# Kernel optimization log

Hardware: AMD Instinct MI355X
Metric: run time of the kernel (lower is better)

The kernel has to match this reference:

```python
import jax, jax.numpy as jnp
import numpy as np

S = 2048      # sequence length (prefill, start_idx=0)
D = 4096      # model dim
H = 32        # query heads
KVH = 8       # kv heads (GQA)
HD = D // H   # head dim = 128
ROPE_BASE = 500000.0  # llama3 rope theta
NEG = -1e9    # additive causal mask value (finite stand-in for -inf)


def setup_inputs() -> dict:
    key = jax.random.key(0)
    ks = jax.random.split(key, 5)
    scale = 1.0 / np.sqrt(D)
    x = jax.random.normal(ks[0], (S, D), jnp.float32)
    wq = jax.random.normal(ks[1], (D, D), jnp.float32) * scale
    wk = jax.random.normal(ks[2], (KVH * HD, D), jnp.float32) * scale
    wv = jax.random.normal(ks[3], (KVH * HD, D), jnp.float32) * scale
    wo = jax.random.normal(ks[4], (D, D), jnp.float32) * scale
    # RoPE tables, [S, HD//2]
    pos = jnp.arange(S, dtype=jnp.float32)
    inv_freq = 1.0 / (ROPE_BASE ** (jnp.arange(0, HD, 2, dtype=jnp.float32) / HD))
    ang = pos[:, None] * inv_freq[None, :]
    freqs_cos = jnp.cos(ang)
    freqs_sin = jnp.sin(ang)
    # additive causal mask [S, S]
    mask = jnp.where(jnp.tril(jnp.ones((S, S), bool)), 0.0, NEG).astype(jnp.float32)
    return dict(x=x, wq=wq, wk=wk, wv=wv, wo=wo, mask=mask,
                freqs_cos=freqs_cos, freqs_sin=freqs_sin)


def _rope(t, cos, sin):
    # t: [S, nh, hd]; cos/sin: [S, hd//2] -> interleaved even/odd rotation
    even = t[:, :, 0::2]
    odd = t[:, :, 1::2]
    c = cos[:, None, :]
    s = sin[:, None, :]
    re = even * c - odd * s
    im = even * s + odd * c
    return jnp.stack([re, im], axis=-1).reshape(t.shape)


def reference(x, wq, wk, wv, wo, mask, freqs_cos, freqs_sin):
    s, d = x.shape
    q = (x @ wq.T).reshape(s, H, HD)
    k = (x @ wk.T).reshape(s, KVH, HD)
    v = (x @ wv.T).reshape(s, KVH, HD)
    q = _rope(q, freqs_cos, freqs_sin)
    k = _rope(k, freqs_cos, freqs_sin)
    # KV-cache append at start_idx=0 then read back == identity (prefill)
    # GQA: repeat_interleave kv heads to match query heads
    k = jnp.repeat(k, H // KVH, axis=1)  # [s, H, HD]
    v = jnp.repeat(v, H // KVH, axis=1)
    logits = jnp.einsum('qhd,khd->hqk', q, k) * (1.0 / np.sqrt(HD)) + mask[None]
    p = jax.nn.softmax(logits, axis=-1)
    o = jnp.einsum('hqk,khd->qhd', p, v).reshape(s, d)
    return o @ wo.T
```

## Files before the change

### kernel.cpp

```cpp
#include <hip/hip_runtime.h>
#include <hip/hip_bf16.h>
#include <stdint.h>

#define S2   2048
#define DD   4096
#define NH   32
#define NKVH 8
#define HD2  128
#define QKVW 6144

typedef __bf16 bf16x8 __attribute__((ext_vector_type(8)));
typedef float  f32x4  __attribute__((ext_vector_type(4)));
typedef unsigned short u16x8 __attribute__((ext_vector_type(8)));
typedef unsigned short u16x4 __attribute__((ext_vector_type(4)));

__device__ __forceinline__ unsigned short f2b(float f) {
    unsigned int u = __builtin_bit_cast(unsigned int, f);
    unsigned int r = (u + 0x7FFFu + ((u >> 16) & 1u)) >> 16;
    return (unsigned short)r;
}
__device__ __forceinline__ float b2f(unsigned short h) {
    unsigned int u = ((unsigned int)h) << 16;
    return __builtin_bit_cast(float, u);
}
__device__ __forceinline__ unsigned cvt_pk_bf16(float a, float b) {
    unsigned r;
    asm("v_cvt_pk_bf16_f32 %0, %1, %2" : "=v"(r) : "v"(a), "v"(b));
    return r;
}

__device__ __forceinline__ void gload_lds16(const void* g, void* lds) {
    __builtin_amdgcn_global_load_lds(
        (const __attribute__((address_space(1))) void*)(uintptr_t)g,
        (__attribute__((address_space(3))) void*)(uint32_t)(uintptr_t)lds,
        16, 0, 0);
}

#define BAR() do { asm volatile("" ::: "memory"); \
                   __builtin_amdgcn_s_barrier();  \
                   asm volatile("" ::: "memory"); } while (0)
#define WAITV(n) asm volatile("s_waitcnt vmcnt(" #n ")" ::: "memory")

template<int N> __device__ __forceinline__ void waitv() {
    if      constexpr (N == 0)  WAITV(0);
    else if constexpr (N == 1)  WAITV(1);
    else if constexpr (N == 2)  WAITV(2);
    else if constexpr (N == 3)  WAITV(3);
    else if constexpr (N == 4)  WAITV(4);
    else if constexpr (N == 5)  WAITV(5);
    else if constexpr (N == 6)  WAITV(6);
    else if constexpr (N == 8)  WAITV(8);
}

__global__ void cvt_all(const float* __restrict__ x,  const float* __restrict__ wq,
                        const float* __restrict__ wk, const float* __restrict__ wv,
                        const float* __restrict__ wo, unsigned short* __restrict__ dst) {
    const long long NG = 12LL * 1024 * 1024;
    const long long stride = (long long)gridDim.x * blockDim.x;
    for (long long g = (long long)blockIdx.x * blockDim.x + threadIdx.x; g < NG; g += stride) {
        const float* src; long long off;
        if      (g < 2LL*1024*1024) { src = x;  off = g; }
        else if (g < 6LL*1024*1024) { src = wq; off = g - 2LL*1024*1024; }
        else if (g < 7LL*1024*1024) { src = wk; off = g - 6LL*1024*1024; }
        else if (g < 8LL*1024*1024) { src = wv; off = g - 7LL*1024*1024; }
        else                        { src = wo; off = g - 8LL*1024*1024; }
        f32x4 v = *reinterpret_cast<const f32x4*>(src + off * 4);
        u16x4 o;
        o[0] = f2b(v[0]); o[1] = f2b(v[1]); o[2] = f2b(v[2]); o[3] = f2b(v[3]);
        *reinterpret_cast<u16x4*>(dst + g * 4) = o;
    }
}

__global__ __launch_bounds__(512) void gemm_qkv(
    const unsigned short* __restrict__ A,
    const unsigned short* __restrict__ B0,
    const unsigned short* __restrict__ B1,
    const unsigned short* __restrict__ B2,
    unsigned short* __restrict__ C)
{
    constexpr int K = 4096, BK = 64, NT = K / BK;
    __shared__ unsigned short As[2][256 * 64];
    __shared__ unsigned short Bs[2][192 * 64];

    const int bm = blockIdx.y, bn = blockIdx.x;
    const int tid = threadIdx.x;
    const int w = tid >> 6, lane = tid & 63;
    const int wr = w >> 1, wc = w & 1;
    const int r16 = lane & 15, g4 = lane >> 4;

    const int bn0 = bn * 192;
    const unsigned short* Ap = A + (size_t)bm * 256 * K;

    const int lrow = lane >> 3;
    const int lchk = lane & 7;

    f32x4 acc[4][6] = {};
    bf16x8 af[2][2], b0[3][2], b1[3][2];

    auto browbase = [&](int rowg) -> const unsigned short* {
        if (rowg < 4096) return B0 + (size_t)rowg * K;
        if (rowg < 5120) return B1 + (size_t)(rowg - 4096) * K;
        return B2 + (size_t)(rowg - 5120) * K;
    };

    auto stageA = [&](int buf, int tt, int half) {
        #pragma unroll
        for (int i = 0; i < 2; ++i) {
            const int j = i * 8 + w;
            const int row0 = (j >> 2) * 64 + half * 32 + (j & 3) * 8;
            const int row = row0 + lrow;
            gload_lds16(Ap + (size_t)row * K + tt * BK + ((lchk ^ (row & 7)) * 8),
                        &As[buf][row0 * 64]);
        }
    };
    auto stageB = [&](int buf, int tt, int half) {
        #pragma unroll
        for (int i = 0; i < 2; ++i) {
            const int j = (i == 0) ? w : (8 + (w & 3));
            const int row0 = (j < 6) ? (half * 48 + j * 8)
                                     : (96 + half * 48 + (j - 6) * 8);
            const int row = row0 + lrow;
            const unsigned short* src = browbase(bn0 + row0) + (size_t)lrow * K;
            gload_lds16(src + tt * BK + ((lchk ^ (row & 7)) * 8),
                        &Bs[buf][row0 * 64]);
        }
    };
    auto readA = [&](int buf, int mh) {
        #pragma unroll
        for (int m = 0; m < 2; ++m)
            #pragma unroll
            for (int kk = 0; kk < 2; ++kk) {
                const int row = wr * 64 + mh * 32 + m * 16 + r16;
                af[m][kk] = *reinterpret_cast<const bf16x8*>(
                    &As[buf][row * 64 + (((kk * 4 + g4) ^ (row & 7)) * 8)]);
            }
    };
    auto readB = [&](int buf, int nh, bf16x8 (&br)[3][2]) {
        #pragma unroll
        for (int n = 0; n < 3; ++n)
            #pragma unroll
            for (int kk = 0; kk < 2; ++kk) {
                const int row = wc * 96 + nh * 48 + n * 16 + r16;
                br[n][kk] = *reinterpret_cast<const bf16x8*>(
                    &Bs[buf][row * 64 + (((kk * 4 + g4) ^ (row & 7)) * 8)]);
            }
    };
    auto mma = [&](bf16x8 (&br)[3][2], int mh, int nh) {
        __builtin_amdgcn_s_setprio(1);
        #pragma unroll
        for (int m = 0; m < 2; ++m)
            #pragma unroll
            for (int n = 0; n < 3; ++n)
                #pragma unroll
                for (int kk = 0; kk < 2; ++kk)
                    acc[mh * 2 + m][nh * 3 + n] = __builtin_amdgcn_mfma_f32_16x16x32_bf16(
                        af[m][kk], br[n][kk], acc[mh * 2 + m][nh * 3 + n], 0, 0, 0);
        __builtin_amdgcn_s_setprio(0);
    };

    stageA(0, 0, 0); stageB(0, 0, 0); stageB(0, 0, 1); stageA(0, 0, 1);
    waitv<4>();
    BAR();

    for (int t = 0; t < NT - 1; ++t) {
        const int buf = t & 1;
        readA(buf, 0); readB(buf, 0, b0);
        stageA(buf ^ 1, t + 1, 0); stageB(buf ^ 1, t + 1, 0);
        BAR();
        mma(b0, 0, 0);
        waitv<6>();
        BAR();
        readB(buf, 1, b1);
        stageB(buf ^ 1, t + 1, 1);
        BAR();
        mma(b1, 0, 1);
        waitv<6>();
        BAR();
        readA(buf, 1);
        stageA(buf ^ 1, t + 1, 1);
        BAR();
        mma(b1, 1, 1);
        BAR();
        mma(b0, 1, 0);
        waitv<4>();
        BAR();
    }
    {
        const int buf = (NT - 1) & 1;
        readA(buf, 0); readB(buf, 0, b0);
        BAR();
        mma(b0, 0, 0);
        waitv<2>();
        BAR();
        readB(buf, 1, b1);
        mma(b1, 0, 1);
        waitv<0>();
        readA(buf, 1);
        mma(b1, 1, 1);
        mma(b0, 1, 0);
    }

    const size_t crow0 = (size_t)bm * 256 + wr * 64;
    const size_t ccol0 = (size_t)bn0 + wc * 96;
    #pragma unroll
    for (int m = 0; m < 4; ++m)
        #pragma unroll
        for (int n = 0; n < 6; ++n)
            #pragma unroll
            for (int r = 0; r < 4; ++r)
                C[(crow0 + m * 16 + g4 * 4 + r) * QKVW + ccol0 + n * 16 + r16] =
                    f2b(acc[m][n][r]);
}

__global__ __launch_bounds__(512) void gemm_out(
    const unsigned short* __restrict__ A,
    const unsigned short* __restrict__ B,
    float* __restrict__ C)
{
    constexpr int K = 4096, BK = 64, NT = K / BK;
    __shared__ unsigned short As[2][128 * 64];
    __shared__ unsigned short Bs[2][256 * 64];

    const int bm = blockIdx.y, bn = blockIdx.x;
    const int tid = threadIdx.x;
    const int w = tid >> 6, lane = tid & 63;
    const int wr = w >> 2, wc = w & 3;
    const int r16 = lane & 15, g4 = lane >> 4;

    const unsigned short* Ap = A + (size_t)bm * 128 * K;
    const unsigned short* Bp = B + (size_t)bn * 256 * K;

    const int lrow = lane >> 3;
    const int lchk = lane & 7;

    f32x4 acc[4][4] = {};
    bf16x8 af[2][2], b0[2][2], b1[2][2];

    auto stageA = [&](int buf, int tt, int half) {
        const int j = w;
        const int row0 = (j >> 2) * 64 + half * 32 + (j & 3) * 8;
        const int row = row0 + lrow;
        gload_lds16(Ap + (size_t)row * K + tt * BK + ((lchk ^ (row & 7)) * 8),
                    &As[buf][row0 * 64]);
    };
    auto stageB = [&](int buf, int tt, int half) {
        #pragma unroll
        for (int i = 0; i < 2; ++i) {
            const int j = i * 8 + w;
            const int row0 = (j >> 2) * 64 + half * 32 + (j & 3) * 8;
            const int row = row0 + lrow;
            gload_lds16(Bp + (size_t)row * K + tt * BK + ((lchk ^ (row & 7)) * 8),
                        &Bs[buf][row0 * 64]);
        }
    };
    auto readA = [&](int buf, int mh) {
        #pragma unroll
        for (int m = 0; m < 2; ++m)
            #pragma unroll
            for (int kk = 0; kk < 2; ++kk) {
                const int row = wr * 64 + mh * 32 + m * 16 + r16;
                af[m][kk] = *reinterpret_cast<const bf16x8*>(
                    &As[buf][row * 64 + (((kk * 4 + g4) ^ (row & 7)) * 8)]);
            }
    };
    auto readB = [&](int buf, int nh, bf16x8 (&br)[2][2]) {
        #pragma unroll
        for (int n = 0; n < 2; ++n)
            #pragma unroll
            for (int kk = 0; kk < 2; ++kk) {
                const int row = wc * 64 + nh * 32 + n * 16 + r16;
                br[n][kk] = *reinterpret_cast<const bf16x8*>(
                    &Bs[buf][row * 64 + (((kk * 4 + g4) ^ (row & 7)) * 8)]);
            }
    };
    auto mma = [&](bf16x8 (&br)[2][2], int mh, int nh) {
        __builtin_amdgcn_s_setprio(1);
        #pragma unroll
        for (int m = 0; m < 2; ++m)
            #pragma unroll
            for (int n = 0; n < 2; ++n)
                #pragma unroll
                for (int kk = 0; kk < 2; ++kk)
                    acc[mh * 2 + m][nh * 2 + n] = __builtin_amdgcn_mfma_f32_16x16x32_bf16(
                        af[m][kk], br[n][kk], acc[mh * 2 + m][nh * 2 + n], 0, 0, 0);
        __builtin_amdgcn_s_setprio(0);
    };

    stageA(0, 0, 0); stageB(0, 0, 0); stageB(0, 0, 1); stageA(0, 0, 1);
    waitv<3>();
    BAR();

    for (int t = 0; t < NT - 1; ++t) {
        const int buf = t & 1;
        readA(buf, 0); readB(buf, 0, b0);
        stageA(buf ^ 1, t + 1, 0); stageB(buf ^ 1, t + 1, 0);
        BAR();
        mma(b0, 0, 0);
        waitv<4>();
        BAR();
        readB(buf, 1, b1);
        stageB(buf ^ 1, t + 1, 1);
        BAR();
        mma(b1, 0, 1);
        waitv<5>();
        BAR();
        readA(buf, 1);
        stageA(buf ^ 1, t + 1, 1);
        BAR();
        mma(b1, 1, 1);
        BAR();
        mma(b0, 1, 0);
        waitv<3>();
        BAR();
    }
    {
        const int buf = (NT - 1) & 1;
        readA(buf, 0); readB(buf, 0, b0);
        BAR();
        mma(b0, 0, 0);
        waitv<1>();
        BAR();
        readB(buf, 1, b1);
        mma(b1, 0, 1);
        waitv<0>();
        readA(buf, 1);
        mma(b1, 1, 1);
        mma(b0, 1, 0);
    }

    const size_t crow0 = (size_t)bm * 128 + wr * 64;
    const size_t ccol0 = (size_t)bn * 256 + wc * 64;
    #pragma unroll
    for (int m = 0; m < 4; ++m)
        #pragma unroll
        for (int n = 0; n < 4; ++n)
            #pragma unroll
            for (int r = 0; r < 4; ++r)
                C[(crow0 + m * 16 + g4 * 4 + r) * DD + ccol0 + n * 16 + r16] = acc[m][n][r];
}

__global__ __launch_bounds__(256) void rope_kernel(unsigned short* __restrict__ qkv,
                                                   const float* __restrict__ fc,
                                                   const float* __restrict__ fs) {
    constexpr float QSCALE = 0.08838834764831845f * 1.4426950408889634f;
    const int g = blockIdx.x * 256 + threadIdx.x;
    if (g >= 640) return;
    const int s = blockIdx.y;
    const int col = g * 8;
    unsigned short* p = qkv + (size_t)s * QKVW + col;
    u16x8 v = *reinterpret_cast<const u16x8*>(p);
    const int i0 = (col & 127) >> 1;
    f32x4 c  = *reinterpret_cast<const f32x4*>(fc + s * 64 + i0);
    f32x4 sn = *reinterpret_cast<const f32x4*>(fs + s * 64 + i0);
    const float post = (col < DD) ? QSCALE : 1.0f;
    u16x8 o;
    #pragma unroll
    for (int j = 0; j < 4; ++j) {
        float e  = b2f(v[2*j]);
        float od = b2f(v[2*j+1]);
        o[2*j]   = f2b((e * c[j] - od * sn[j]) * post);
        o[2*j+1] = f2b((e * sn[j] + od * c[j]) * post);
    }
    *reinterpret_cast<u16x8*>(p) = o;
}

__global__ __launch_bounds__(256) void transpose_v(const unsigned short* __restrict__ qkv,
                                                   unsigned short* __restrict__ Vt) {
    __shared__ unsigned short tile[64][72];
    const int d0g = blockIdx.x * 64;
    const int s0  = blockIdx.y * 64;
    const int kvh = d0g >> 7, dl0 = d0g & 127;
    const int tid = threadIdx.x;
    #pragma unroll
    for (int p = 0; p < 2; ++p) {
        const int sgi = p * 256 + tid;
        const int srow = sgi >> 3, dseg = sgi & 7;
        u16x8 v = *reinterpret_cast<const u16x8*>(
            qkv + (size_t)(s0 + srow) * QKVW + 5120 + d0g + dseg * 8);
        #pragma unroll
        for (int j = 0; j < 8; ++j) tile[srow][dseg * 8 + j] = v[j];
    }
    __syncthreads();
    #pragma unroll
    for (int p = 0; p < 2; ++p) {
        const int sgi = p * 256 + tid;
        const int drow = sgi >> 3, sseg = sgi & 7;
        u16x8 v;
        #pragma unroll
        for (int j = 0; j < 8; ++j) v[j] = tile[sseg * 8 + j][drow];
        *reinterpret_cast<u16x8*>(
            Vt + (size_t)kvh * HD2 * S2 + (size_t)(dl0 + drow) * S2 + s0 + sseg * 8) = v;
    }
}

__global__ __launch_bounds__(512) void attn_kernel(const unsigned short* __restrict__ Qkv,
                                                   const unsigned short* __restrict__ Vt,
                                                   unsigned short* __restrict__ O) {
    __shared__ unsigned short Klds[2][64 * 128];
    __shared__ unsigned short Vlds[2][128 * 64];
    __shared__ unsigned short Plds[8][2048];

    const int kvh = blockIdx.x;
    const int h   = kvh * 4 + (blockIdx.y & 3);
    const int p   = blockIdx.y >> 2;
    const int cB  = 8 + p, cS = 7 - p;
    const int w = threadIdx.x >> 6, lane = threadIdx.x & 63;
    const int r16 = lane & 15, g4 = lane >> 4;

    const int myc = (w < 4) ? cB : cS;
    const int qw  = myc * 128 + (w & 3) * 32;
    const int ntB = 2 * cB + 2;

    const unsigned short* Kbase = Qkv + DD + kvh * HD2;
    const unsigned short* Vtb   = Vt + (size_t)kvh * HD2 * S2;
    char* pw = (char*)(&Plds[w][0]);

    const int krow_l = lane >> 4;
    const int kchunk = lane & 15;
    const int vd_l   = lane >> 3;
    const int vchunk = lane & 7;

    bf16x8 qf[2][4];
    #pragma unroll
    for (int m = 0; m < 2; ++m)
        #pragma unroll
        for (int f = 0; f < 4; ++f)
            qf[m][f] = *reinterpret_cast<const bf16x8*>(
                Qkv + (size_t)(qw + m * 16 + r16) * QKVW + h * HD2 + f * 32 + g4 * 8);

    f32x4 o[2][8] = {};
    float mr[2] = {-3e38f, -3e38f};
    float lr[2] = {0.f, 0.f};

    auto stage = [&](int buf, int kv0) {
        #pragma unroll
        for (int i = 0; i < 2; ++i) {
            const int seg = i * 8 + w;
            const int row = seg * 4 + krow_l;
            gload_lds16(Kbase + (size_t)(kv0 + row) * QKVW + ((kchunk ^ (row & 7)) * 8),
                        &Klds[buf][seg * 512]);
        }
        #pragma unroll
        for (int i = 0; i < 2; ++i) {
            const int seg = i * 8 + w;
            const int d = seg * 8 + vd_l;
            gload_lds16(Vtb + (size_t)d * S2 + kv0 + ((vchunk ^ (d & 7)) * 8),
                        &Vlds[buf][seg * 512]);
        }
    };

    stage(0, 0);
    WAITV(0);
    __syncthreads();

    for (int t = 0; t < ntB; ++t) {
        const int buf = t & 1;
        const int kv0 = t * 64;
        if (t + 1 < ntB) stage(buf ^ 1, (t + 1) * 64);

        if (kv0 <= qw + 31) {
            f32x4 sa[2][4] = {};
            #pragma unroll
            for (int kb = 0; kb < 4; ++kb) {
                bf16x8 kf[4];
                #pragma unroll
                for (int f = 0; f < 4; ++f)
                    kf[f] = *reinterpret_cast<const bf16x8*>(
                        &Klds[buf][(kb * 16 + r16) * 128 + (((f * 4 + g4) ^ (r16 & 7)) * 8)]);
                __builtin_amdgcn_s_setprio(1);
                #pragma unroll
                for (int m = 0; m < 2; ++m)
                    #pragma unroll
                    for (int f = 0; f < 4; ++f)
                        sa[m][kb] = __builtin_amdgcn_mfma_f32_16x16x32_bf16(
                            kf[f], qf[m][f], sa[m][kb], 0, 0, 0);
                __builtin_amdgcn_s_setprio(0);
            }
            const bool needmask = (kv0 + 63 > qw);
            float sv[2][4][4];
            #pragma unroll
            for (int m = 0; m < 2; ++m)
                #pragma unroll
                for (int kb = 0; kb < 4; ++kb)
                    #pragma unroll
                    for (int r = 0; r < 4; ++r) {
                        float xx = sa[m][kb][r];
                        if (needmask) {
                            const int kvg = kv0 + kb * 16 + g4 * 4 + r;
                            const int qg  = qw + m * 16 + r16;
                            xx = (kvg > qg) ? -3e38f : xx;
                        }
                        sv[m][kb][r] = xx;
                    }
            float rowm[2];
            #pragma unroll
            for (int m = 0; m < 2; ++m) {
                float a0 = fmaxf(fmaxf(sv[m][0][0], sv[m][0][1]), fmaxf(sv[m][0][2], sv[m][0][3]));
                float a1 = fmaxf(fmaxf(sv[m][1][0], sv[m][1][1]), fmaxf(sv[m][1][2], sv[m][1][3]));
                float a2 = fmaxf(fmaxf(sv[m][2][0], sv[m][2][1]), fmaxf(sv[m][2][2], sv[m][2][3]));
                float a3 = fmaxf(fmaxf(sv[m][3][0], sv[m][3][1]), fmaxf(sv[m][3][2], sv[m][3][3]));
                rowm[m] = fmaxf(fmaxf(a0, a1), fmaxf(a2, a3));
            }
            #pragma unroll
            for (int m = 0; m < 2; ++m) {
                rowm[m] = fmaxf(rowm[m], __shfl_xor(rowm[m], 16));
                rowm[m] = fmaxf(rowm[m], __shfl_xor(rowm[m], 32));
            }
            const float gmax = fmaxf(rowm[0] - mr[0], rowm[1] - mr[1]);
            if (!__all(gmax <= 11.5f)) {
                float corr[2];
                #pragma unroll
                for (int m = 0; m < 2; ++m) {
                    const float mn = fmaxf(mr[m], rowm[m]);
                    corr[m] = exp2f(mr[m] - mn);
                    mr[m] = mn;
                    lr[m] *= corr[m];
                }
                #pragma unroll
                for (int m = 0; m < 2; ++m)
                    #pragma unroll
                    for (int r = 0; r < 4; ++r) {
                        const float co = __shfl(corr[m], (lane & 48) | (g4 * 4 + r));
                        #pragma unroll
                        for (int n = 0; n < 8; ++n) o[m][n][r] *= co;
                    }
            }
            float rs[2] = {0.f, 0.f};
            #pragma unroll
            for (int m = 0; m < 2; ++m)
                #pragma unroll
                for (int kb = 0; kb < 4; ++kb)
                    #pragma unroll
                    for (int r = 0; r < 4; ++r) {
                        const float pp = exp2f(sv[m][kb][r] - mr[m]);
                        sv[m][kb][r] = pp;
                        rs[m] += pp;
                    }
            #pragma unroll
            for (int m = 0; m < 2; ++m) {
                rs[m] += __shfl_xor(rs[m], 16);
                rs[m] += __shfl_xor(rs[m], 32);
                lr[m] += rs[m];
            }
            #pragma unroll
            for (int m = 0; m < 2; ++m)
                #pragma unroll
                for (int kb = 0; kb < 4; ++kb) {
                    const unsigned w0 = cvt_pk_bf16(sv[m][kb][0], sv[m][kb][1]);
                    const unsigned w1 = cvt_pk_bf16(sv[m][kb][2], sv[m][kb][3]);
                    int wa = m * 2048 + ((kb * 2) + (g4 >> 1)) * 256 + r16 * 16 + (g4 & 1) * 8;
                    wa ^= (r16 >> 3) << 4;
                    *reinterpret_cast<unsigned long long*>(pw + wa) =
                        (unsigned long long)w0 | ((unsigned long long)w1 << 32);
                }
            asm volatile("s_waitcnt lgkmcnt(0)" ::: "memory");
            bf16x8 pa[2][2];
            #pragma unroll
            for (int m = 0; m < 2; ++m)
                #pragma unroll
                for (int kvs = 0; kvs < 2; ++kvs) {
                    int ra = m * 2048 + kvs * 1024 + lane * 16;
                    ra ^= (r16 >> 3) << 4;
                    pa[m][kvs] = *reinterpret_cast<const bf16x8*>(pw + ra);
                }
            #pragma unroll
            for (int kvs = 0; kvs < 2; ++kvs)
                #pragma unroll
                for (int n = 0; n < 8; ++n) {
                    const bf16x8 vb = *reinterpret_cast<const bf16x8*>(
                        &Vlds[buf][(n * 16 + r16) * 64 + (((kvs * 4 + g4) ^ (r16 & 7)) * 8)]);
                    __builtin_amdgcn_s_setprio(1);
                    #pragma unroll
                    for (int m = 0; m < 2; ++m)
                        o[m][n] = __builtin_amdgcn_mfma_f32_16x16x32_bf16(
                            pa[m][kvs], vb, o[m][n], 0, 0, 0);
                    __builtin_amdgcn_s_setprio(0);
                }
        }

        WAITV(0);
        __syncthreads();
    }

    float inv[2];
    #pragma unroll
    for (int m = 0; m < 2; ++m) inv[m] = 1.0f / lr[m];
    #pragma unroll
    for (int m = 0; m < 2; ++m)
        #pragma unroll
        for (int r = 0; r < 4; ++r) {
            const float iv = __shfl(inv[m], (lane & 48) | (g4 * 4 + r));
            #pragma unroll
            for (int n = 0; n < 8; ++n)
                O[(size_t)(qw + m * 16 + g4 * 4 + r) * DD + h * HD2 + n * 16 + r16] =
                    f2b(o[m][n][r] * iv);
        }
}

extern "C" void kernel_launch(void* const* d_in, const int* in_sizes, int n_in,
                              void* d_out, int out_size, void* d_ws, size_t ws_size,
                              hipStream_t stream) {
    (void)in_sizes; (void)n_in; (void)out_size; (void)ws_size;
    const float* x  = (const float*)d_in[0];
    const float* wq = (const float*)d_in[1];
    const float* wk = (const float*)d_in[2];
    const float* wv = (const float*)d_in[3];
    const float* wo = (const float*)d_in[4];
    const float* fc = (const float*)d_in[6];
    const float* fs = (const float*)d_in[7];
    float* out = (float*)d_out;

    unsigned short* ws = (unsigned short*)d_ws;
    const size_t M1 = 1024 * 1024;
    unsigned short* xb  = ws;
    unsigned short* wqb = ws + 8  * M1;
    unsigned short* wkb = ws + 24 * M1;
    unsigned short* wvb = ws + 28 * M1;
    unsigned short* wob = ws + 32 * M1;
    unsigned short* qkv = ws + 48 * M1;
    unsigned short* vt  = ws + 60 * M1;
    unsigned short* ob  = ws + 62 * M1;

    cvt_all<<<2048, 256, 0, stream>>>(x, wq, wk, wv, wo, ws);
    gemm_qkv<<<dim3(32, 8), 512, 0, stream>>>(xb, wqb, wkb, wvb, qkv);
    rope_kernel<<<dim3(3, 2048), 256, 0, stream>>>(qkv, fc, fs);
    transpose_v<<<dim3(16, 32), 256, 0, stream>>>(qkv, vt);
    attn_kernel<<<dim3(8, 32), 512, 0, stream>>>(qkv, vt, ob);
    gemm_out<<<dim3(16, 16), 512, 0, stream>>>(ob, wob, out);
}
```

Measured before the change: 299.7 us.

## Use 12-wave QKV GEMM blocks and triple-buffer K/V tiles in attention

The QKV GEMM moves from 8 waves (4x2, each 64x96) to 12 waves (4x3, each 64x64) per 256x192 tile. Each wave now holds fewer accumulators, and the global-to-LDS staging and wait counts are adjusted to match. The attention kernel switches from double to triple buffering of K/V tiles, prefetching two tiles ahead to hide load latency. In exchange it uses more LDS per block, which may reduce occupancy, and the GEMM blocks pay more barrier cost with more waves.

```diff
diff --git a/kernel.cpp b/kernel.cpp
--- a/kernel.cpp
+++ b/kernel.cpp
@@ -71,7 +71,7 @@
     }
 }
 
-__global__ __launch_bounds__(512) void gemm_qkv(
+__global__ __launch_bounds__(768) void gemm_qkv(
     const unsigned short* __restrict__ A,
     const unsigned short* __restrict__ B0,
     const unsigned short* __restrict__ B1,
@@ -85,7 +85,7 @@
     const int bm = blockIdx.y, bn = blockIdx.x;
     const int tid = threadIdx.x;
     const int w = tid >> 6, lane = tid & 63;
-    const int wr = w >> 1, wc = w & 1;
+    const int wr = w / 3, wc = w % 3;
     const int r16 = lane & 15, g4 = lane >> 4;
 
     const int bn0 = bn * 192;
@@ -94,8 +94,8 @@
     const int lrow = lane >> 3;
     const int lchk = lane & 7;
 
-    f32x4 acc[4][6] = {};
-    bf16x8 af[2][2], b0[3][2], b1[3][2];
+    f32x4 acc[4][4] = {};
+    bf16x8 af[2][2], b0[2][2], b1[2][2];
 
     auto browbase = [&](int rowg) -> const unsigned short* {
         if (rowg < 4096) return B0 + (size_t)rowg * K;
@@ -106,24 +106,20 @@
     auto stageA = [&](int buf, int tt, int half) {
         #pragma unroll
         for (int i = 0; i < 2; ++i) {
-            const int j = i * 8 + w;
-            const int row0 = (j >> 2) * 64 + half * 32 + (j & 3) * 8;
+            const int j = (i == 0) ? w : (12 + (w & 3));
+            const int row0 = (j & 3) * 8 + (j >> 2) * 64 + half * 32;
             const int row = row0 + lrow;
             gload_lds16(Ap + (size_t)row * K + tt * BK + ((lchk ^ (row & 7)) * 8),
                         &As[buf][row0 * 64]);
         }
     };
     auto stageB = [&](int buf, int tt, int half) {
-        #pragma unroll
-        for (int i = 0; i < 2; ++i) {
-            const int j = (i == 0) ? w : (8 + (w & 3));
-            const int row0 = (j < 6) ? (half * 48 + j * 8)
-                                     : (96 + half * 48 + (j - 6) * 8);
-            const int row = row0 + lrow;
-            const unsigned short* src = browbase(bn0 + row0) + (size_t)lrow * K;
-            gload_lds16(src + tt * BK + ((lchk ^ (row & 7)) * 8),
-                        &Bs[buf][row0 * 64]);
-        }
+        const int j = w;
+        const int row0 = (j & 3) * 8 + (j >> 2) * 64 + half * 32;
+        const int row = row0 + lrow;
+        const unsigned short* src = browbase(bn0 + row0) + (size_t)lrow * K;
+        gload_lds16(src + tt * BK + ((lchk ^ (row & 7)) * 8),
+                    &Bs[buf][row0 * 64]);
     };
     auto readA = [&](int buf, int mh) {
         #pragma unroll
@@ -135,31 +131,31 @@
                     &As[buf][row * 64 + (((kk * 4 + g4) ^ (row & 7)) * 8)]);
             }
     };
-    auto readB = [&](int buf, int nh, bf16x8 (&br)[3][2]) {
-        #pragma unroll
-        for (int n = 0; n < 3; ++n)
+    auto readB = [&](int buf, int nh, bf16x8 (&br)[2][2]) {
+        #pragma unroll
+        for (int n = 0; n < 2; ++n)
             #pragma unroll
             for (int kk = 0; kk < 2; ++kk) {
-                const int row = wc * 96 + nh * 48 + n * 16 + r16;
+                const int row = wc * 64 + nh * 32 + n * 16 + r16;
                 br[n][kk] = *reinterpret_cast<const bf16x8*>(
                     &Bs[buf][row * 64 + (((kk * 4 + g4) ^ (row & 7)) * 8)]);
             }
     };
-    auto mma = [&](bf16x8 (&br)[3][2], int mh, int nh) {
+    auto mma = [&](bf16x8 (&br)[2][2], int mh, int nh) {
         __builtin_amdgcn_s_setprio(1);
         #pragma unroll
         for (int m = 0; m < 2; ++m)
             #pragma unroll
-            for (int n = 0; n < 3; ++n)
+            for (int n = 0; n < 2; ++n)
                 #pragma unroll
                 for (int kk = 0; kk < 2; ++kk)
-                    acc[mh * 2 + m][nh * 3 + n] = __builtin_amdgcn_mfma_f32_16x16x32_bf16(
-                        af[m][kk], br[n][kk], acc[mh * 2 + m][nh * 3 + n], 0, 0, 0);
+                    acc[mh * 2 + m][nh * 2 + n] = __builtin_amdgcn_mfma_f32_16x16x32_bf16(
+                        af[m][kk], br[n][kk], acc[mh * 2 + m][nh * 2 + n], 0, 0, 0);
         __builtin_amdgcn_s_setprio(0);
     };
 
     stageA(0, 0, 0); stageB(0, 0, 0); stageB(0, 0, 1); stageA(0, 0, 1);
-    waitv<4>();
+    waitv<3>();
     BAR();
 
     for (int t = 0; t < NT - 1; ++t) {
@@ -168,13 +164,13 @@
         stageA(buf ^ 1, t + 1, 0); stageB(buf ^ 1, t + 1, 0);
         BAR();
         mma(b0, 0, 0);
-        waitv<6>();
+        waitv<5>();
         BAR();
         readB(buf, 1, b1);
         stageB(buf ^ 1, t + 1, 1);
         BAR();
         mma(b1, 0, 1);
-        waitv<6>();
+        waitv<4>();
         BAR();
         readA(buf, 1);
         stageA(buf ^ 1, t + 1, 1);
@@ -182,7 +178,7 @@
         mma(b1, 1, 1);
         BAR();
         mma(b0, 1, 0);
-        waitv<4>();
+        waitv<3>();
         BAR();
     }
     {
@@ -201,15 +197,21 @@
     }
 
     const size_t crow0 = (size_t)bm * 256 + wr * 64;
-    const size_t ccol0 = (size_t)bn0 + wc * 96;
-    #pragma unroll
-    for (int m = 0; m < 4; ++m)
-        #pragma unroll
-        for (int n = 0; n < 6; ++n)
-            #pragma unroll
-            for (int r = 0; r < 4; ++r)
-                C[(crow0 + m * 16 + g4 * 4 + r) * QKVW + ccol0 + n * 16 + r16] =
-                    f2b(acc[m][n][r]);
+    const size_t ccol0 = (size_t)bn0 + wc * 64;
+    #pragma unroll
+    for (int mh = 0; mh < 2; ++mh)
+        #pragma unroll
+        for (int m = 0; m < 2; ++m)
+            #pragma unroll
+            for (int nh = 0; nh < 2; ++nh)
+                #pragma unroll
+                for (int n = 0; n < 2; ++n)
+                    #pragma unroll
+                    for (int r = 0; r < 4; ++r) {
+                        const size_t row = crow0 + mh * 32 + m * 16 + g4 * 4 + r;
+                        const size_t col = ccol0 + nh * 32 + n * 16 + r16;
+                        C[row * QKVW + col] = f2b(acc[mh * 2 + m][nh * 2 + n][r]);
+                    }
 }
 
 __global__ __launch_bounds__(512) void gemm_out(
@@ -396,8 +398,8 @@
 __global__ __launch_bounds__(512) void attn_kernel(const unsigned short* __restrict__ Qkv,
                                                    const unsigned short* __restrict__ Vt,
                                                    unsigned short* __restrict__ O) {
-    __shared__ unsigned short Klds[2][64 * 128];
-    __shared__ unsigned short Vlds[2][128 * 64];
+    __shared__ unsigned short Klds[3][64 * 128];
+    __shared__ unsigned short Vlds[3][128 * 64];
     __shared__ unsigned short Plds[8][2048];
 
     const int kvh = blockIdx.x;
@@ -432,31 +434,32 @@
     float mr[2] = {-3e38f, -3e38f};
     float lr[2] = {0.f, 0.f};
 
-    auto stage = [&](int buf, int kv0) {
+    auto stage = [&](int slot, int kv0) {
         #pragma unroll
         for (int i = 0; i < 2; ++i) {
             const int seg = i * 8 + w;
             const int row = seg * 4 + krow_l;
             gload_lds16(Kbase + (size_t)(kv0 + row) * QKVW + ((kchunk ^ (row & 7)) * 8),
-                        &Klds[buf][seg * 512]);
+                        &Klds[slot][seg * 512]);
         }
         #pragma unroll
         for (int i = 0; i < 2; ++i) {
             const int seg = i * 8 + w;
             const int d = seg * 8 + vd_l;
             gload_lds16(Vtb + (size_t)d * S2 + kv0 + ((vchunk ^ (d & 7)) * 8),
-                        &Vlds[buf][seg * 512]);
+                        &Vlds[slot][seg * 512]);
         }
     };
 
     stage(0, 0);
-    WAITV(0);
+    stage(1, 64);
+    WAITV(4);
     __syncthreads();
 
+    int rs = 0, ws2 = 2;
     for (int t = 0; t < ntB; ++t) {
-        const int buf = t & 1;
         const int kv0 = t * 64;
-        if (t + 1 < ntB) stage(buf ^ 1, (t + 1) * 64);
+        if (t + 2 < ntB) stage(ws2, (t + 2) * 64);
 
         if (kv0 <= qw + 31) {
             f32x4 sa[2][4] = {};
@@ -466,7 +469,7 @@
                 #pragma unroll
                 for (int f = 0; f < 4; ++f)
                     kf[f] = *reinterpret_cast<const bf16x8*>(
-                        &Klds[buf][(kb * 16 + r16) * 128 + (((f * 4 + g4) ^ (r16 & 7)) * 8)]);
+                        &Klds[rs][(kb * 16 + r16) * 128 + (((f * 4 + g4) ^ (r16 & 7)) * 8)]);
                 __builtin_amdgcn_s_setprio(1);
                 #pragma unroll
                 for (int m = 0; m < 2; ++m)
@@ -525,7 +528,7 @@
                         for (int n = 0; n < 8; ++n) o[m][n][r] *= co;
                     }
             }
-            float rs[2] = {0.f, 0.f};
+            float rsum[2] = {0.f, 0.f};
             #pragma unroll
             for (int m = 0; m < 2; ++m)
                 #pragma unroll
@@ -534,13 +537,13 @@
                     for (int r = 0; r < 4; ++r) {
                         const float pp = exp2f(sv[m][kb][r] - mr[m]);
                         sv[m][kb][r] = pp;
-                        rs[m] += pp;
+                        rsum[m] += pp;
                     }
             #pragma unroll
             for (int m = 0; m < 2; ++m) {
-                rs[m] += __shfl_xor(rs[m], 16);
-                rs[m] += __shfl_xor(rs[m], 32);
-                lr[m] += rs[m];
+                rsum[m] += __shfl_xor(rsum[m], 16);
+                rsum[m] += __shfl_xor(rsum[m], 32);
+                lr[m] += rsum[m];
             }
             #pragma unroll
             for (int m = 0; m < 2; ++m)
@@ -568,7 +571,7 @@
                 #pragma unroll
                 for (int n = 0; n < 8; ++n) {
                     const bf16x8 vb = *reinterpret_cast<const bf16x8*>(
-                        &Vlds[buf][(n * 16 + r16) * 64 + (((kvs * 4 + g4) ^ (r16 & 7)) * 8)]);
+                        &Vlds[rs][(n * 16 + r16) * 64 + (((kvs * 4 + g4) ^ (r16 & 7)) * 8)]);
                     __builtin_amdgcn_s_setprio(1);
                     #pragma unroll
                     for (int m = 0; m < 2; ++m)
@@ -578,8 +581,10 @@
                 }
         }
 
-        WAITV(0);
+        if (t + 2 < ntB) { WAITV(4); } else { WAITV(0); }
         __syncthreads();
+        rs  = (rs  == 2) ? 0 : rs  + 1;
+        ws2 = (ws2 == 2) ? 0 : ws2 + 1;
     }
 
     float inv[2];
@@ -622,7 +627,7 @@
     unsigned short* ob  = ws + 62 * M1;
 
     cvt_all<<<2048, 256, 0, stream>>>(x, wq, wk, wv, wo, ws);
-    gemm_qkv<<<dim3(32, 8), 512, 0, stream>>>(xb, wqb, wkb, wvb, qkv);
+    gemm_qkv<<<dim3(32, 8), 768, 0, stream>>>(xb, wqb, wkb, wvb, qkv);
     rope_kernel<<<dim3(3, 2048), 256, 0, stream>>>(qkv, fc, fs);
     transpose_v<<<dim3(16, 32), 256, 0, stream>>>(qkv, vt);
     attn_kernel<<<dim3(8, 32), 512, 0, stream>>>(qkv, vt, ob);
```

New measurement: 301.8 us. Within noise of the previous version (+0.7%).

## Process KV tiles in pairs with quad-buffered LDS and one softmax update

Applied to the files above, without the earlier changes.

The attention loop now stages two 64-row KV tiles per iteration into a four-slot LDS ring instead of one tile into a double buffer. Both QK^T products are computed before a single shared max/rescale and row-sum reduction, and then both PV products run. This halves the barrier and wait count per KV and amortizes the online-softmax bookkeeping. In exchange it doubles K/V LDS usage, which may reduce occupancy, and raises register pressure from holding two score tiles at once.

```diff
diff --git a/kernel.cpp b/kernel.cpp
--- a/kernel.cpp
+++ b/kernel.cpp
@@ -396,8 +396,8 @@
 __global__ __launch_bounds__(512) void attn_kernel(const unsigned short* __restrict__ Qkv,
                                                    const unsigned short* __restrict__ Vt,
                                                    unsigned short* __restrict__ O) {
-    __shared__ unsigned short Klds[2][64 * 128];
-    __shared__ unsigned short Vlds[2][128 * 64];
+    __shared__ unsigned short Klds[4][64 * 128];
+    __shared__ unsigned short Vlds[4][128 * 64];
     __shared__ unsigned short Plds[8][2048];
 
     const int kvh = blockIdx.x;
@@ -409,7 +409,7 @@
 
     const int myc = (w < 4) ? cB : cS;
     const int qw  = myc * 128 + (w & 3) * 32;
-    const int ntB = 2 * cB + 2;
+    const int np  = cB + 1;
 
     const unsigned short* Kbase = Qkv + DD + kvh * HD2;
     const unsigned short* Vtb   = Vt + (size_t)kvh * HD2 * S2;
@@ -432,74 +432,133 @@
     float mr[2] = {-3e38f, -3e38f};
     float lr[2] = {0.f, 0.f};
 
-    auto stage = [&](int buf, int kv0) {
-        #pragma unroll
-        for (int i = 0; i < 2; ++i) {
-            const int seg = i * 8 + w;
-            const int row = seg * 4 + krow_l;
-            gload_lds16(Kbase + (size_t)(kv0 + row) * QKVW + ((kchunk ^ (row & 7)) * 8),
-                        &Klds[buf][seg * 512]);
+    auto stagePair = [&](int slot0, int kv0) {
+        #pragma unroll
+        for (int tt = 0; tt < 2; ++tt) {
+            const int slot = slot0 + tt;
+            const int kvb = kv0 + tt * 64;
+            #pragma unroll
+            for (int i = 0; i < 2; ++i) {
+                const int seg = i * 8 + w;
+                const int row = seg * 4 + krow_l;
+                gload_lds16(Kbase + (size_t)(kvb + row) * QKVW + ((kchunk ^ (row & 7)) * 8),
+                            &Klds[slot][seg * 512]);
+            }
+            #pragma unroll
+            for (int i = 0; i < 2; ++i) {
+                const int seg = i * 8 + w;
+                const int d = seg * 8 + vd_l;
+                gload_lds16(Vtb + (size_t)d * S2 + kvb + ((vchunk ^ (d & 7)) * 8),
+                            &Vlds[slot][seg * 512]);
+            }
         }
-        #pragma unroll
-        for (int i = 0; i < 2; ++i) {
-            const int seg = i * 8 + w;
-            const int d = seg * 8 + vd_l;
-            gload_lds16(Vtb + (size_t)d * S2 + kv0 + ((vchunk ^ (d & 7)) * 8),
-                        &Vlds[buf][seg * 512]);
+    };
+
+    auto qkt = [&](int slot, int kvb, float (&svt)[2][4][4]) {
+        f32x4 sa[2][4] = {};
+        #pragma unroll
+        for (int kb = 0; kb < 4; ++kb) {
+            bf16x8 kf[4];
+            #pragma unroll
+            for (int f = 0; f < 4; ++f)
+                kf[f] = *reinterpret_cast<const bf16x8*>(
+                    &Klds[slot][(kb * 16 + r16) * 128 + (((f * 4 + g4) ^ (r16 & 7)) * 8)]);
+            __builtin_amdgcn_s_setprio(1);
+            #pragma unroll
+            for (int m = 0; m < 2; ++m)
+                #pragma unroll
+                for (int f = 0; f < 4; ++f)
+                    sa[m][kb] = __builtin_amdgcn_mfma_f32_16x16x32_bf16(
+                        kf[f], qf[m][f], sa[m][kb], 0, 0, 0);
+            __builtin_amdgcn_s_setprio(0);
         }
-    };
-
-    stage(0, 0);
+        const bool needmask = (kvb + 63 > qw);
+        #pragma unroll
+        for (int m = 0; m < 2; ++m)
+            #pragma unroll
+            for (int kb = 0; kb < 4; ++kb)
+                #pragma unroll
+                for (int r = 0; r < 4; ++r) {
+                    float xx = sa[m][kb][r];
+                    if (needmask) {
+                        const int kvg = kvb + kb * 16 + g4 * 4 + r;
+                        const int qg  = qw + m * 16 + r16;
+                        xx = (kvg > qg) ? -3e38f : xx;
+                    }
+                    svt[m][kb][r] = xx;
+                }
+    };
+
+    auto pv = [&](int slot, float (&svt)[2][4][4]) {
+        #pragma unroll
+        for (int m = 0; m < 2; ++m)
+            #pragma unroll
+            for (int kb = 0; kb < 4; ++kb) {
+                const unsigned w0 = cvt_pk_bf16(svt[m][kb][0], svt[m][kb][1]);
+                const unsigned w1 = cvt_pk_bf16(svt[m][kb][2], svt[m][kb][3]);
+                int wa = m * 2048 + ((kb * 2) + (g4 >> 1)) * 256 + r16 * 16 + (g4 & 1) * 8;
+                wa ^= (r16 >> 3) << 4;
+                *reinterpret_cast<unsigned long long*>(pw + wa) =
+                    (unsigned long long)w0 | ((unsigned long long)w1 << 32);
+            }
+        asm volatile("s_waitcnt lgkmcnt(0)" ::: "memory");
+        bf16x8 pa[2][2];
+        #pragma unroll
+        for (int m = 0; m < 2; ++m)
+            #pragma unroll
+            for (int kvs = 0; kvs < 2; ++kvs) {
+                int ra = m * 2048 + kvs * 1024 + lane * 16;
+                ra ^= (r16 >> 3) << 4;
+                pa[m][kvs] = *reinterpret_cast<const bf16x8*>(pw + ra);
+            }
+        #pragma unroll
+        for (int kvs = 0; kvs < 2; ++kvs)
+            #pragma unroll
+            for (int n = 0; n < 8; ++n) {
+                const bf16x8 vb = *reinterpret_cast<const bf16x8*>(
+                    &Vlds[slot][(n * 16 + r16) * 64 + (((kvs * 4 + g4) ^ (r16 & 7)) * 8)]);
+                __builtin_amdgcn_s_setprio(1);
+                #pragma unroll
+                for (int m = 0; m < 2; ++m)
+                    o[m][n] = __builtin_amdgcn_mfma_f32_16x16x32_bf16(
+                        pa[m][kvs], vb, o[m][n], 0, 0, 0);
+                __builtin_amdgcn_s_setprio(0);
+            }
+    };
+
+    stagePair(0, 0);
     WAITV(0);
     __syncthreads();
 
-    for (int t = 0; t < ntB; ++t) {
-        const int buf = t & 1;
-        const int kv0 = t * 64;
-        if (t + 1 < ntB) stage(buf ^ 1, (t + 1) * 64);
+    for (int j = 0; j < np; ++j) {
+        const int s0 = (j & 1) * 2;
+        const int kv0 = j * 128;
+        if (j + 1 < np) stagePair(s0 ^ 2, kv0 + 128);
 
         if (kv0 <= qw + 31) {
-            f32x4 sa[2][4] = {};
-            #pragma unroll
-            for (int kb = 0; kb < 4; ++kb) {
-                bf16x8 kf[4];
-                #pragma unroll
-                for (int f = 0; f < 4; ++f)
-                    kf[f] = *reinterpret_cast<const bf16x8*>(
-                        &Klds[buf][(kb * 16 + r16) * 128 + (((f * 4 + g4) ^ (r16 & 7)) * 8)]);
-                __builtin_amdgcn_s_setprio(1);
-                #pragma unroll
-                for (int m = 0; m < 2; ++m)
-                    #pragma unroll
-                    for (int f = 0; f < 4; ++f)
-                        sa[m][kb] = __builtin_amdgcn_mfma_f32_16x16x32_bf16(
-                            kf[f], qf[m][f], sa[m][kb], 0, 0, 0);
-                __builtin_amdgcn_s_setprio(0);
-            }
-            const bool needmask = (kv0 + 63 > qw);
-            float sv[2][4][4];
-            #pragma unroll
-            for (int m = 0; m < 2; ++m)
-                #pragma unroll
-                for (int kb = 0; kb < 4; ++kb)
-                    #pragma unroll
-                    for (int r = 0; r < 4; ++r) {
-                        float xx = sa[m][kb][r];
-                        if (needmask) {
-                            const int kvg = kv0 + kb * 16 + g4 * 4 + r;
-                            const int qg  = qw + m * 16 + r16;
-                            xx = (kvg > qg) ? -3e38f : xx;
-                        }
-                        sv[m][kb][r] = xx;
-                    }
+            const bool have1 = (kv0 + 64 <= qw + 31);
+            float sv0[2][4][4], sv1[2][4][4];
+            qkt(s0, kv0, sv0);
+            if (have1) qkt(s0 + 1, kv0 + 64, sv1);
+
             float rowm[2];
             #pragma unroll
             for (int m = 0; m < 2; ++m) {
-                float a0 = fmaxf(fmaxf(sv[m][0][0], sv[m][0][1]), fmaxf(sv[m][0][2], sv[m][0][3]));
-                float a1 = fmaxf(fmaxf(sv[m][1][0], sv[m][1][1]), fmaxf(sv[m][1][2], sv[m][1][3]));
-                float a2 = fmaxf(fmaxf(sv[m][2][0], sv[m][2][1]), fmaxf(sv[m][2][2], sv[m][2][3]));
-                float a3 = fmaxf(fmaxf(sv[m][3][0], sv[m][3][1]), fmaxf(sv[m][3][2], sv[m][3][3]));
+                float a0 = fmaxf(fmaxf(sv0[m][0][0], sv0[m][0][1]), fmaxf(sv0[m][0][2], sv0[m][0][3]));
+                float a1 = fmaxf(fmaxf(sv0[m][1][0], sv0[m][1][1]), fmaxf(sv0[m][1][2], sv0[m][1][3]));
+                float a2 = fmaxf(fmaxf(sv0[m][2][0], sv0[m][2][1]), fmaxf(sv0[m][2][2], sv0[m][2][3]));
+                float a3 = fmaxf(fmaxf(sv0[m][3][0], sv0[m][3][1]), fmaxf(sv0[m][3][2], sv0[m][3][3]));
                 rowm[m] = fmaxf(fmaxf(a0, a1), fmaxf(a2, a3));
+            }
+            if (have1) {
+                #pragma unroll
+                for (int m = 0; m < 2; ++m) {
+                    float a0 = fmaxf(fmaxf(sv1[m][0][0], sv1[m][0][1]), fmaxf(sv1[m][0][2], sv1[m][0][3]));
+                    float a1 = fmaxf(fmaxf(sv1[m][1][0], sv1[m][1][1]), fmaxf(sv1[m][1][2], sv1[m][1][3]));
+                    float a2 = fmaxf(fmaxf(sv1[m][2][0], sv1[m][2][1]), fmaxf(sv1[m][2][2], sv1[m][2][3]));
+                    float a3 = fmaxf(fmaxf(sv1[m][3][0], sv1[m][3][1]), fmaxf(sv1[m][3][2], sv1[m][3][3]));
+                    rowm[m] = fmaxf(rowm[m], fmaxf(fmaxf(a0, a1), fmaxf(a2, a3)));
+                }
             }
             #pragma unroll
             for (int m = 0; m < 2; ++m) {
@@ -525,57 +584,37 @@
                         for (int n = 0; n < 8; ++n) o[m][n][r] *= co;
                     }
             }
-            float rs[2] = {0.f, 0.f};
+            float rsum[2] = {0.f, 0.f};
             #pragma unroll
             for (int m = 0; m < 2; ++m)
                 #pragma unroll
                 for (int kb = 0; kb < 4; ++kb)
                     #pragma unroll
                     for (int r = 0; r < 4; ++r) {
-                        const float pp = exp2f(sv[m][kb][r] - mr[m]);
-                        sv[m][kb][r] = pp;
-                        rs[m] += pp;
+                        const float pp = exp2f(sv0[m][kb][r] - mr[m]);
+                        sv0[m][kb][r] = pp;
+                        rsum[m] += pp;
                     }
+            if (have1) {
+                #pragma unroll
+                for (int m = 0; m < 2; ++m)
+                    #pragma unroll
+                    for (int kb = 0; kb < 4; ++kb)
+                        #pragma unroll
+                        for (int r = 0; r < 4; ++r) {
+                            const float pp = exp2f(sv1[m][kb][r] - mr[m]);
+                            sv1[m][kb][r] = pp;
+                            rsum[m] += pp;
+                        }
+            }
             #pragma unroll
             for (int m = 0; m < 2; ++m) {
-                rs[m] += __shfl_xor(rs[m], 16);
-                rs[m] += __shfl_xor(rs[m], 32);
-                lr[m] += rs[m];
-            }
-            #pragma unroll
-            for (int m = 0; m < 2; ++m)
-                #pragma unroll
-                for (int kb = 0; kb < 4; ++kb) {
-                    const unsigned w0 = cvt_pk_bf16(sv[m][kb][0], sv[m][kb][1]);
-                    const unsigned w1 = cvt_pk_bf16(sv[m][kb][2], sv[m][kb][3]);
-                    int wa = m * 2048 + ((kb * 2) + (g4 >> 1)) * 256 + r16 * 16 + (g4 & 1) * 8;
-                    wa ^= (r16 >> 3) << 4;
-                    *reinterpret_cast<unsigned long long*>(pw + wa) =
-                        (unsigned long long)w0 | ((unsigned long long)w1 << 32);
-                }
-            asm volatile("s_waitcnt lgkmcnt(0)" ::: "memory");
-            bf16x8 pa[2][2];
-            #pragma unroll
-            for (int m = 0; m < 2; ++m)
-                #pragma unroll
-                for (int kvs = 0; kvs < 2; ++kvs) {
-                    int ra = m * 2048 + kvs * 1024 + lane * 16;
-                    ra ^= (r16 >> 3) << 4;
-                    pa[m][kvs] = *reinterpret_cast<const bf16x8*>(pw + ra);
-                }
-            #pragma unroll
-            for (int kvs = 0; kvs < 2; ++kvs)
-                #pragma unroll
-                for (int n = 0; n < 8; ++n) {
-                    const bf16x8 vb = *reinterpret_cast<const bf16x8*>(
-                        &Vlds[buf][(n * 16 + r16) * 64 + (((kvs * 4 + g4) ^ (r16 & 7)) * 8)]);
-                    __builtin_amdgcn_s_setprio(1);
-                    #pragma unroll
-                    for (int m = 0; m < 2; ++m)
-                        o[m][n] = __builtin_amdgcn_mfma_f32_16x16x32_bf16(
-                            pa[m][kvs], vb, o[m][n], 0, 0, 0);
-                    __builtin_amdgcn_s_setprio(0);
-                }
+                rsum[m] += __shfl_xor(rsum[m], 16);
+                rsum[m] += __shfl_xor(rsum[m], 32);
+                lr[m] += rsum[m];
+            }
+            pv(s0, sv0);
+            if (have1) pv(s0 + 1, sv1);
         }
 
         WAITV(0);
```

Result: no change. 300.5 us (+0.3%).

## Overlap wo bf16 conversion with attention and merge rope with V transpose

Applied to the files above, without the earlier changes.

Moves the fp32-to-bf16 conversion of the output projection weight out of the upfront conversion kernel and into the attention kernel. There it is issued as register-staged loads across the first few KV iterations, so it hides under attention compute. Also merges the RoPE and V-transpose kernels into one launch, removing a kernel boundary. In exchange, attention carries extra register pressure and memory traffic that may lower occupancy or slow its pipeline.

```diff
diff --git a/kernel.cpp b/kernel.cpp
--- a/kernel.cpp
+++ b/kernel.cpp
@@ -54,16 +54,15 @@
 
 __global__ void cvt_all(const float* __restrict__ x,  const float* __restrict__ wq,
                         const float* __restrict__ wk, const float* __restrict__ wv,
-                        const float* __restrict__ wo, unsigned short* __restrict__ dst) {
-    const long long NG = 12LL * 1024 * 1024;
+                        unsigned short* __restrict__ dst) {
+    const long long NG = 8LL * 1024 * 1024;
     const long long stride = (long long)gridDim.x * blockDim.x;
     for (long long g = (long long)blockIdx.x * blockDim.x + threadIdx.x; g < NG; g += stride) {
         const float* src; long long off;
         if      (g < 2LL*1024*1024) { src = x;  off = g; }
         else if (g < 6LL*1024*1024) { src = wq; off = g - 2LL*1024*1024; }
         else if (g < 7LL*1024*1024) { src = wk; off = g - 6LL*1024*1024; }
-        else if (g < 8LL*1024*1024) { src = wv; off = g - 7LL*1024*1024; }
-        else                        { src = wo; off = g - 8LL*1024*1024; }
+        else                        { src = wv; off = g - 7LL*1024*1024; }
         f32x4 v = *reinterpret_cast<const f32x4*>(src + off * 4);
         u16x4 o;
         o[0] = f2b(v[0]); o[1] = f2b(v[1]); o[2] = f2b(v[2]); o[3] = f2b(v[3]);
@@ -339,63 +338,67 @@
                 C[(crow0 + m * 16 + g4 * 4 + r) * DD + ccol0 + n * 16 + r16] = acc[m][n][r];
 }
 
-__global__ __launch_bounds__(256) void rope_kernel(unsigned short* __restrict__ qkv,
-                                                   const float* __restrict__ fc,
-                                                   const float* __restrict__ fs) {
-    constexpr float QSCALE = 0.08838834764831845f * 1.4426950408889634f;
-    const int g = blockIdx.x * 256 + threadIdx.x;
-    if (g >= 640) return;
-    const int s = blockIdx.y;
-    const int col = g * 8;
-    unsigned short* p = qkv + (size_t)s * QKVW + col;
-    u16x8 v = *reinterpret_cast<const u16x8*>(p);
-    const int i0 = (col & 127) >> 1;
-    f32x4 c  = *reinterpret_cast<const f32x4*>(fc + s * 64 + i0);
-    f32x4 sn = *reinterpret_cast<const f32x4*>(fs + s * 64 + i0);
-    const float post = (col < DD) ? QSCALE : 1.0f;
-    u16x8 o;
-    #pragma unroll
-    for (int j = 0; j < 4; ++j) {
-        float e  = b2f(v[2*j]);
-        float od = b2f(v[2*j+1]);
-        o[2*j]   = f2b((e * c[j] - od * sn[j]) * post);
-        o[2*j+1] = f2b((e * sn[j] + od * c[j]) * post);
-    }
-    *reinterpret_cast<u16x8*>(p) = o;
-}
-
-__global__ __launch_bounds__(256) void transpose_v(const unsigned short* __restrict__ qkv,
-                                                   unsigned short* __restrict__ Vt) {
+__global__ __launch_bounds__(256) void rope_tv(unsigned short* __restrict__ qkv,
+                                               const float* __restrict__ fc,
+                                               const float* __restrict__ fs,
+                                               unsigned short* __restrict__ Vt) {
     __shared__ unsigned short tile[64][72];
-    const int d0g = blockIdx.x * 64;
-    const int s0  = blockIdx.y * 64;
-    const int kvh = d0g >> 7, dl0 = d0g & 127;
-    const int tid = threadIdx.x;
-    #pragma unroll
-    for (int p = 0; p < 2; ++p) {
-        const int sgi = p * 256 + tid;
-        const int srow = sgi >> 3, dseg = sgi & 7;
-        u16x8 v = *reinterpret_cast<const u16x8*>(
-            qkv + (size_t)(s0 + srow) * QKVW + 5120 + d0g + dseg * 8);
-        #pragma unroll
-        for (int j = 0; j < 8; ++j) tile[srow][dseg * 8 + j] = v[j];
-    }
-    __syncthreads();
-    #pragma unroll
-    for (int p = 0; p < 2; ++p) {
-        const int sgi = p * 256 + tid;
-        const int drow = sgi >> 3, sseg = sgi & 7;
-        u16x8 v;
-        #pragma unroll
-        for (int j = 0; j < 8; ++j) v[j] = tile[sseg * 8 + j][drow];
-        *reinterpret_cast<u16x8*>(
-            Vt + (size_t)kvh * HD2 * S2 + (size_t)(dl0 + drow) * S2 + s0 + sseg * 8) = v;
+    const int bid = blockIdx.x;
+    if (bid < 6144) {
+        constexpr float QSCALE = 0.08838834764831845f * 1.4426950408889634f;
+        const int g = (bid % 3) * 256 + threadIdx.x;
+        if (g >= 640) return;
+        const int s = bid / 3;
+        const int col = g * 8;
+        unsigned short* p = qkv + (size_t)s * QKVW + col;
+        u16x8 v = *reinterpret_cast<const u16x8*>(p);
+        const int i0 = (col & 127) >> 1;
+        f32x4 c  = *reinterpret_cast<const f32x4*>(fc + s * 64 + i0);
+        f32x4 sn = *reinterpret_cast<const f32x4*>(fs + s * 64 + i0);
+        const float post = (col < DD) ? QSCALE : 1.0f;
+        u16x8 o;
+        #pragma unroll
+        for (int j = 0; j < 4; ++j) {
+            float e  = b2f(v[2*j]);
+            float od = b2f(v[2*j+1]);
+            o[2*j]   = f2b((e * c[j] - od * sn[j]) * post);
+            o[2*j+1] = f2b((e * sn[j] + od * c[j]) * post);
+        }
+        *reinterpret_cast<u16x8*>(p) = o;
+    } else {
+        const int t = bid - 6144;
+        const int d0g = (t & 15) * 64;
+        const int s0  = (t >> 4) * 64;
+        const int kvh = d0g >> 7, dl0 = d0g & 127;
+        const int tid = threadIdx.x;
+        #pragma unroll
+        for (int p = 0; p < 2; ++p) {
+            const int sgi = p * 256 + tid;
+            const int srow = sgi >> 3, dseg = sgi & 7;
+            u16x8 v = *reinterpret_cast<const u16x8*>(
+                qkv + (size_t)(s0 + srow) * QKVW + 5120 + d0g + dseg * 8);
+            #pragma unroll
+            for (int j = 0; j < 8; ++j) tile[srow][dseg * 8 + j] = v[j];
+        }
+        __syncthreads();
+        #pragma unroll
+        for (int p = 0; p < 2; ++p) {
+            const int sgi = p * 256 + tid;
+            const int drow = sgi >> 3, sseg = sgi & 7;
+            u16x8 v;
+            #pragma unroll
+            for (int j = 0; j < 8; ++j) v[j] = tile[sseg * 8 + j][drow];
+            *reinterpret_cast<u16x8*>(
+                Vt + (size_t)kvh * HD2 * S2 + (size_t)(dl0 + drow) * S2 + s0 + sseg * 8) = v;
+        }
     }
 }
 
 __global__ __launch_bounds__(512) void attn_kernel(const unsigned short* __restrict__ Qkv,
                                                    const unsigned short* __restrict__ Vt,
-                                                   unsigned short* __restrict__ O) {
+                                                   unsigned short* __restrict__ O,
+                                                   const float* __restrict__ wo_src,
+                                                   unsigned short* __restrict__ wo_dst) {
     __shared__ unsigned short Klds[2][64 * 128];
     __shared__ unsigned short Vlds[2][128 * 64];
     __shared__ unsigned short Plds[8][2048];
@@ -405,6 +408,7 @@
     const int p   = blockIdx.y >> 2;
     const int cB  = 8 + p, cS = 7 - p;
     const int w = threadIdx.x >> 6, lane = threadIdx.x & 63;
+    const int tid = threadIdx.x;
     const int r16 = lane & 15, g4 = lane >> 4;
 
     const int myc = (w < 4) ? cB : cS;
@@ -414,6 +418,25 @@
     const unsigned short* Kbase = Qkv + DD + kvh * HD2;
     const unsigned short* Vtb   = Vt + (size_t)kvh * HD2 * S2;
     char* pw = (char*)(&Plds[w][0]);
+
+    const int blk = blockIdx.y * 8 + blockIdx.x;
+    const f32x4* wo4 = (const f32x4*)wo_src;
+    const int cb4 = blk * 16384 + tid;
+    f32x4 cbuf[8];
+    auto cvt_issue = [&](int k) {
+        #pragma unroll
+        for (int i = 0; i < 8; ++i)
+            cbuf[i] = wo4[cb4 + k * 4096 + i * 512];
+    };
+    auto cvt_flush = [&](int k) {
+        #pragma unroll
+        for (int i = 0; i < 8; ++i) {
+            u16x4 ov;
+            ov[0] = f2b(cbuf[i][0]); ov[1] = f2b(cbuf[i][1]);
+            ov[2] = f2b(cbuf[i][2]); ov[3] = f2b(cbuf[i][3]);
+            *reinterpret_cast<u16x4*>(wo_dst + ((size_t)(cb4 + k * 4096 + i * 512)) * 4) = ov;
+        }
+    };
 
     const int krow_l = lane >> 4;
     const int kchunk = lane & 15;
@@ -452,8 +475,13 @@
     stage(0, 0);
     WAITV(0);
     __syncthreads();
+    cvt_issue(0);
 
     for (int t = 0; t < ntB; ++t) {
+        if (t >= 1 && t <= 4) {
+            cvt_flush(t - 1);
+            if (t < 4) cvt_issue(t);
+        }
         const int buf = t & 1;
         const int kv0 = t * 64;
         if (t + 1 < ntB) stage(buf ^ 1, (t + 1) * 64);
@@ -621,10 +649,9 @@
     unsigned short* vt  = ws + 60 * M1;
     unsigned short* ob  = ws + 62 * M1;
 
-    cvt_all<<<2048, 256, 0, stream>>>(x, wq, wk, wv, wo, ws);
+    cvt_all<<<2048, 256, 0, stream>>>(x, wq, wk, wv, ws);
     gemm_qkv<<<dim3(32, 8), 512, 0, stream>>>(xb, wqb, wkb, wvb, qkv);
-    rope_kernel<<<dim3(3, 2048), 256, 0, stream>>>(qkv, fc, fs);
-    transpose_v<<<dim3(16, 32), 256, 0, stream>>>(qkv, vt);
-    attn_kernel<<<dim3(8, 32), 512, 0, stream>>>(qkv, vt, ob);
+    rope_tv<<<6656, 256, 0, stream>>>(qkv, fc, fs, vt);
+    attn_kernel<<<dim3(8, 32), 512, 0, stream>>>(qkv, vt, ob, wo, wob);
     gemm_out<<<dim3(16, 16), 512, 0, stream>>>(ob, wob, out);
 }
```

Measured after the change: 294.0 us. Within noise of the previous version (-1.9%).
